# Performance work log

Measured on AMD Instinct MI355X. Metric: run time of the kernel, lower is better.

The kernel has to match this reference:

```python
import jax, jax.numpy as jnp
import numpy as np

B, R, M, L, H = 256, 2048, 65536, 64, 4  # batch, reservoir, memory_size, key_len, read_heads


def setup_inputs() -> dict:
    key = jax.random.key(0)
    ks = jax.random.split(key, 4)
    s = 1.0 / np.sqrt(R).astype(np.float32)  # ~xavier scale for Linear weights
    return {
        "reservoir_state": jax.random.normal(ks[0], (B, R), dtype=jnp.float32),
        "memory": jax.random.normal(ks[1], (1, M, L), dtype=jnp.float32),
        "Wk": jax.random.normal(ks[2], (H * L, R), dtype=jnp.float32) * s,
        "bk": jnp.zeros((H * L,), dtype=jnp.float32),
        "Wb": jax.random.normal(ks[3], (H, R), dtype=jnp.float32) * s,
        "bb": jnp.zeros((H,), dtype=jnp.float32),
    }


def reference(reservoir_state, memory, Wk, bk, Wb, bb):
    b = reservoir_state.shape[0]
    h = Wb.shape[0]
    # key projection -> [B, H, L]
    keys = (reservoir_state @ Wk.T + bk).reshape(b, h, -1)
    # per-head key strength, relu-gated -> [B, H]
    betas = jax.nn.relu(reservoir_state @ Wb.T + bb)
    # content addressing: dot(keys, memory rows) -> [B, H, M]
    dots = jnp.einsum('bhl,ml->bhm', keys, memory[0])
    # normalize by key norm (as in original: sqrt(sum(keys^2)))
    dots = dots / jnp.sqrt(jnp.sum(keys ** 2, axis=-1, keepdims=True))
    # beta-scaled softmax over memory slots
    return jax.nn.softmax(betas[:, :, None] * dots, axis=-1)
```

## Files before the change

### kernel.cpp

```cpp
#include <hip/hip_runtime.h>
#include <hip/hip_bf16.h>

#define BB   256
#define RR   2048
#define MM   65536
#define LL   64
#define HH   4
#define NROW 1024
#define KEYS 256

typedef float f32x4 __attribute__((ext_vector_type(4)));
typedef short short8 __attribute__((ext_vector_type(8)));

#define MFMA(A,B,C) __builtin_amdgcn_mfma_f32_16x16x32_bf16((A),(B),(C),0,0,0)

__device__ __forceinline__ unsigned short bf16_rn(float x) {
    union { float f; unsigned int u; } v; v.f = x;
    unsigned int r = v.u + 0x7FFFu + ((v.u >> 16) & 1u);
    return (unsigned short)(r >> 16);
}
__device__ __forceinline__ float bf16_to_f(unsigned short h) {
    union { float f; unsigned int u; } v; v.u = ((unsigned int)h) << 16; return v.f;
}
__device__ __forceinline__ void split8_store(const float* x, unsigned short* hi, unsigned short* lo) {
    unsigned int ph[4], pl[4];
#pragma unroll
    for (int j = 0; j < 4; ++j) {
        unsigned short h0 = bf16_rn(x[2*j]),   l0 = bf16_rn(x[2*j]   - bf16_to_f(h0));
        unsigned short h1 = bf16_rn(x[2*j+1]), l1 = bf16_rn(x[2*j+1] - bf16_to_f(h1));
        ph[j] = (unsigned int)h0 | ((unsigned int)h1 << 16);
        pl[j] = (unsigned int)l0 | ((unsigned int)l1 << 16);
    }
    ((uint4*)hi)[0] = make_uint4(ph[0], ph[1], ph[2], ph[3]);
    ((uint4*)lo)[0] = make_uint4(pl[0], pl[1], pl[2], pl[3]);
}

__global__ __launch_bounds__(256) void transpose_k(const float* __restrict__ in,
                                                   float* __restrict__ out,
                                                   int NR, int NC) {
    __shared__ float t[64 * 65];
    int r0 = blockIdx.x * 64, c0 = blockIdx.y * 64;
    int lane = threadIdx.x & 63, w = threadIdx.x >> 6;
#pragma unroll
    for (int i = 0; i < 16; ++i) {
        int rr = i * 4 + w;
        t[lane * 65 + rr] = in[(size_t)(r0 + rr) * NC + c0 + lane];
    }
    __syncthreads();
#pragma unroll
    for (int i = 0; i < 16; ++i) {
        int cc = i * 4 + w;
        out[(size_t)(c0 + cc) * NR + r0 + lane] = t[cc * 65 + lane];
    }
}

__global__ __launch_bounds__(256) void normmax_k(const float* __restrict__ mem,
                                                 float* __restrict__ normpart) {
    int row = blockIdx.x * 256 + threadIdx.x;
    const float4* p = (const float4*)(mem + (size_t)row * LL);
    float s = 0.f;
#pragma unroll
    for (int i = 0; i < 16; ++i) { float4 v = p[i]; s += v.x*v.x + v.y*v.y + v.z*v.z + v.w*v.w; }
    int lane = threadIdx.x & 63, w = threadIdx.x >> 6;
#pragma unroll
    for (int off = 1; off < 64; off <<= 1) s = fmaxf(s, __shfl_xor(s, off, 64));
    __shared__ float sm[4];
    if (lane == 0) sm[w] = s;
    __syncthreads();
    if (threadIdx.x == 0)
        normpart[blockIdx.x] = fmaxf(fmaxf(sm[0], sm[1]), fmaxf(sm[2], sm[3]));
}

__global__ __launch_bounds__(256) void prep_mem(const float* __restrict__ mem,
                                                unsigned short* __restrict__ bhi,
                                                unsigned short* __restrict__ blo) {
    int gid = blockIdx.x * 256 + threadIdx.x;
    int lane = gid & 63, frag = gid >> 6;
    int t = frag >> 1, c = frag & 1;
    int mrow = t * 16 + (lane & 15);
    int k0 = c * 32 + (lane >> 4) * 8;
    const float4* src = (const float4*)(mem + (size_t)mrow * LL + k0);
    float4 x0 = src[0], x1 = src[1];
    float x[8] = {x0.x, x0.y, x0.z, x0.w, x1.x, x1.y, x1.z, x1.w};
    split8_store(x, bhi + (size_t)gid * 8, blo + (size_t)gid * 8);
}

__global__ __launch_bounds__(256) void k0_keys(const float* __restrict__ S,
                                               const float* __restrict__ WkT,
                                               float* __restrict__ kpart) {
    __shared__ float sl[8 * 256];
    int bg = blockIdx.x, kc = blockIdx.y, tid = threadIdx.x;
    int b0 = bg * 8;
#pragma unroll
    for (int bi = 0; bi < 8; ++bi)
        sl[bi * 256 + tid] = S[(size_t)(b0 + bi) * RR + kc * 256 + tid];
    __syncthreads();
    float acc[8] = {0,0,0,0,0,0,0,0};
    const float* wp = WkT + (size_t)kc * 256 * KEYS + tid;
#pragma unroll 4
    for (int kk = 0; kk < 256; ++kk) {
        float wv = wp[kk * KEYS];
#pragma unroll
        for (int bi = 0; bi < 8; ++bi)
            acc[bi] = fmaf(sl[bi * 256 + kk], wv, acc[bi]);
    }
    float* op = kpart + (size_t)kc * BB * KEYS + (size_t)b0 * KEYS + tid;
#pragma unroll
    for (int bi = 0; bi < 8; ++bi)
        op[bi * KEYS] = acc[bi];
}

__global__ __launch_bounds__(256) void k1_finalize(const float* __restrict__ S,
                                                   const float* __restrict__ kpart,
                                                   const float* __restrict__ bk,
                                                   const float* __restrict__ Wb,
                                                   const float* __restrict__ bb,
                                                   const float* __restrict__ normpart,
                                                   float* __restrict__ q_rm,
                                                   float* __restrict__ brow) {
    int bh = blockIdx.x, b = bh >> 2, h = bh & 3;
    int tid = threadIdx.x, lane = tid & 63, w = tid >> 6;
    float p = 0.f;
#pragma unroll
    for (int i = 0; i < 8; ++i) {
        int k = i * 256 + tid;
        p += S[(size_t)b * RR + k] * Wb[(size_t)h * RR + k];
    }
    float nm = normpart[tid];
#pragma unroll
    for (int off = 1; off < 64; off <<= 1) {
        p  += __shfl_xor(p, off, 64);
        nm  = fmaxf(nm, __shfl_xor(nm, off, 64));
    }
    __shared__ float red[4], redm[4];
    if (lane == 0) { red[w] = p; redm[w] = nm; }
    __syncthreads();
    if (tid < 64) {
        float beta = red[0] + red[1] + red[2] + red[3] + bb[h];
        beta = fmaxf(beta, 0.f);
        float maxn = sqrtf(fmaxf(fmaxf(redm[0], redm[1]), fmaxf(redm[2], redm[3])));
        float kv = bk[h * LL + lane];
#pragma unroll
        for (int c = 0; c < 8; ++c)
            kv += kpart[(size_t)c * BB * KEYS + (size_t)b * KEYS + h * LL + lane];
        float sq = kv * kv;
#pragma unroll
        for (int off = 1; off < 64; off <<= 1) sq += __shfl_xor(sq, off, 64);
        float scale = beta / sqrtf(sq);
        q_rm[(size_t)bh * LL + lane] = kv * scale;
        if (lane == 0) brow[bh] = beta * maxn;
    }
}

__global__ __launch_bounds__(256) void prep_a(const float* __restrict__ q_rm,
                                              unsigned short* __restrict__ ahi,
                                              unsigned short* __restrict__ alo) {
    int gid = blockIdx.x * 256 + threadIdx.x;
    int lane = gid & 63, frag = gid >> 6;
    int rtg = frag >> 1, c = frag & 1;
    int row = rtg * 16 + (lane & 15);
    int k0 = c * 32 + (lane >> 4) * 8;
    const float4* src = (const float4*)(q_rm + (size_t)row * LL + k0);
    float4 x0 = src[0], x1 = src[1];
    float x[8] = {x0.x, x0.y, x0.z, x0.w, x1.x, x1.y, x1.z, x1.w};
    split8_store(x, ahi + (size_t)gid * 8, alo + (size_t)gid * 8);
}

__global__ __launch_bounds__(256) void k2_mfma(const unsigned short* __restrict__ bhi,
                                               const unsigned short* __restrict__ blo,
                                               const unsigned short* __restrict__ ahi,
                                               const unsigned short* __restrict__ alo,
                                               const float* __restrict__ brow,
                                               float* __restrict__ psum) {
    int bx = blockIdx.x;
    int mblk = bx >> 4, rg = bx & 15;
    int tid = threadIdx.x, w = tid >> 6, lane = tid & 63;
    int g = lane >> 4;
    short8 Ah[4][2], Al[4][2];
#pragma unroll
    for (int rt = 0; rt < 4; ++rt)
#pragma unroll
        for (int c = 0; c < 2; ++c) {
            size_t off = ((size_t)((rg * 4 + rt) * 2 + c) * 64 + lane) * 8;
            Ah[rt][c] = *(const short8*)(ahi + off);
            Al[rt][c] = *(const short8*)(alo + off);
        }
    float br[4][4];
#pragma unroll
    for (int rt = 0; rt < 4; ++rt)
#pragma unroll
        for (int r = 0; r < 4; ++r)
            br[rt][r] = brow[rg * 64 + rt * 16 + g * 4 + r];
    float s[4][4] = {{0.f}};
    int t0 = mblk * 64 + w * 16;
    for (int ti = 0; ti < 16; ++ti) {
        int t = t0 + ti;
        size_t o0 = ((size_t)(t * 2 + 0) * 64 + lane) * 8;
        size_t o1 = ((size_t)(t * 2 + 1) * 64 + lane) * 8;
        short8 Bh0 = *(const short8*)(bhi + o0);
        short8 Bh1 = *(const short8*)(bhi + o1);
        short8 Bl0 = *(const short8*)(blo + o0);
        short8 Bl1 = *(const short8*)(blo + o1);
#pragma unroll
        for (int rt = 0; rt < 4; ++rt) {
            f32x4 C = {0.f, 0.f, 0.f, 0.f};
            C = MFMA(Ah[rt][0], Bh0, C);
            C = MFMA(Ah[rt][1], Bh1, C);
            C = MFMA(Al[rt][0], Bh0, C);
            C = MFMA(Al[rt][1], Bh1, C);
            C = MFMA(Ah[rt][0], Bl0, C);
            C = MFMA(Ah[rt][1], Bl1, C);
#pragma unroll
            for (int r = 0; r < 4; ++r)
                s[rt][r] += __expf(C[r] - br[rt][r]);
        }
    }
#pragma unroll
    for (int rt = 0; rt < 4; ++rt)
#pragma unroll
        for (int r = 0; r < 4; ++r) {
            float v = s[rt][r];
            v += __shfl_xor(v, 1, 64);
            v += __shfl_xor(v, 2, 64);
            v += __shfl_xor(v, 4, 64);
            v += __shfl_xor(v, 8, 64);
            s[rt][r] = v;
        }
    if ((lane & 15) == 0) {
        int col = mblk * 4 + w;
#pragma unroll
        for (int rt = 0; rt < 4; ++rt)
#pragma unroll
            for (int r = 0; r < 4; ++r) {
                int row = rg * 64 + rt * 16 + g * 4 + r;
                psum[(size_t)row * 256 + col] = s[rt][r];
            }
    }
}

__global__ __launch_bounds__(256) void k3_combine(const float* __restrict__ psum,
                                                  float* __restrict__ ginv) {
    int row = blockIdx.x, tid = threadIdx.x, lane = tid & 63, w = tid >> 6;
    float v = psum[(size_t)row * 256 + tid];
#pragma unroll
    for (int off = 1; off < 64; off <<= 1) v += __shfl_xor(v, off, 64);
    __shared__ float sm[4];
    if (lane == 0) sm[w] = v;
    __syncthreads();
    if (tid == 0) ginv[row] = 1.0f / (sm[0] + sm[1] + sm[2] + sm[3]);
}

__global__ __launch_bounds__(256) void k4_mfma(const unsigned short* __restrict__ bhi,
                                               const unsigned short* __restrict__ blo,
                                               const unsigned short* __restrict__ ahi,
                                               const unsigned short* __restrict__ alo,
                                               const float* __restrict__ brow,
                                               const float* __restrict__ ginv,
                                               float* __restrict__ out) {
    int bx = blockIdx.x;
    int mblk = bx >> 4, rg = bx & 15;
    int tid = threadIdx.x, w = tid >> 6, lane = tid & 63;
    int g = lane >> 4;
    short8 Ah[4][2], Al[4][2];
#pragma unroll
    for (int rt = 0; rt < 4; ++rt)
#pragma unroll
        for (int c = 0; c < 2; ++c) {
            size_t off = ((size_t)((rg * 4 + rt) * 2 + c) * 64 + lane) * 8;
            Ah[rt][c] = *(const short8*)(ahi + off);
            Al[rt][c] = *(const short8*)(alo + off);
        }
    float br[4][4], gv[4][4];
    size_t rbase[4][4];
#pragma unroll
    for (int rt = 0; rt < 4; ++rt)
#pragma unroll
        for (int r = 0; r < 4; ++r) {
            int row = rg * 64 + rt * 16 + g * 4 + r;
            br[rt][r] = brow[row];
            gv[rt][r] = ginv[row];
            rbase[rt][r] = (size_t)row * MM + (lane & 15);
        }
    int t0 = mblk * 64 + w * 16;
    for (int ti = 0; ti < 16; ++ti) {
        int t = t0 + ti;
        size_t o0 = ((size_t)(t * 2 + 0) * 64 + lane) * 8;
        size_t o1 = ((size_t)(t * 2 + 1) * 64 + lane) * 8;
        short8 Bh0 = *(const short8*)(bhi + o0);
        short8 Bh1 = *(const short8*)(bhi + o1);
        short8 Bl0 = *(const short8*)(blo + o0);
        short8 Bl1 = *(const short8*)(blo + o1);
#pragma unroll
        for (int rt = 0; rt < 4; ++rt) {
            f32x4 C = {0.f, 0.f, 0.f, 0.f};
            C = MFMA(Ah[rt][0], Bh0, C);
            C = MFMA(Ah[rt][1], Bh1, C);
            C = MFMA(Al[rt][0], Bh0, C);
            C = MFMA(Al[rt][1], Bh1, C);
            C = MFMA(Ah[rt][0], Bl0, C);
            C = MFMA(Ah[rt][1], Bl1, C);
#pragma unroll
            for (int r = 0; r < 4; ++r) {
                float o = __expf(C[r] - br[rt][r]) * gv[rt][r];
                __builtin_nontemporal_store(o, out + rbase[rt][r] + (size_t)t * 16);
            }
        }
    }
}

extern "C" void kernel_launch(void* const* d_in, const int* in_sizes, int n_in,
                              void* d_out, int out_size, void* d_ws, size_t ws_size,
                              hipStream_t stream) {
    const float* S   = (const float*)d_in[0];
    const float* mem = (const float*)d_in[1];
    const float* Wk  = (const float*)d_in[2];
    const float* bk  = (const float*)d_in[3];
    const float* Wb  = (const float*)d_in[4];
    const float* bb  = (const float*)d_in[5];
    float* out = (float*)d_out;

    float* WkT      = (float*)d_ws;
    float* kpart    = WkT   + (size_t)RR * KEYS;
    float* q_rm     = kpart + (size_t)8 * BB * KEYS;
    float* psum     = q_rm  + (size_t)NROW * LL;
    float* brow     = psum  + (size_t)NROW * 256;
    float* ginv     = brow  + NROW;
    float* normpart = ginv  + NROW;
    unsigned short* bhi = (unsigned short*)(normpart + 256);
    unsigned short* blo = bhi + (size_t)8192 * 512;
    unsigned short* ahi = blo + (size_t)8192 * 512;
    unsigned short* alo = ahi + (size_t)128 * 512;

    transpose_k<<<dim3(BB / 64, RR / 64), 256, 0, stream>>>(Wk, WkT, KEYS, RR);
    normmax_k  <<<256,         256, 0, stream>>>(mem, normpart);
    prep_mem   <<<2048,        256, 0, stream>>>(mem, bhi, blo);
    k0_keys    <<<dim3(32, 8), 256, 0, stream>>>(S, WkT, kpart);
    k1_finalize<<<NROW,        256, 0, stream>>>(S, kpart, bk, Wb, bb, normpart, q_rm, brow);
    prep_a     <<<32,          256, 0, stream>>>(q_rm, ahi, alo);
    k2_mfma    <<<1024,        256, 0, stream>>>(bhi, blo, ahi, alo, brow, psum);
    k3_combine <<<NROW,        256, 0, stream>>>(psum, ginv);
    k4_mfma    <<<1024,        256, 0, stream>>>(bhi, blo, ahi, alo, brow, ginv, out);
}
```

Baseline: 397.3 us.

## Fuse norm-max into prep_mem, stage output via LDS, prefetch B, use exp2

```diff
diff --git a/kernel.cpp b/kernel.cpp
--- a/kernel.cpp
+++ b/kernel.cpp
@@ -13,6 +13,8 @@
 typedef short short8 __attribute__((ext_vector_type(8)));
 
 #define MFMA(A,B,C) __builtin_amdgcn_mfma_f32_16x16x32_bf16((A),(B),(C),0,0,0)
+#define LOG2E 1.4426950408889634f
+#define EXP2F(x) __builtin_amdgcn_exp2f(x)
 
 __device__ __forceinline__ unsigned short bf16_rn(float x) {
     union { float f; unsigned int u; } v; v.f = x;
@@ -54,35 +56,49 @@
     }
 }
 
-__global__ __launch_bounds__(256) void normmax_k(const float* __restrict__ mem,
-                                                 float* __restrict__ normpart) {
-    int row = blockIdx.x * 256 + threadIdx.x;
-    const float4* p = (const float4*)(mem + (size_t)row * LL);
-    float s = 0.f;
-#pragma unroll
-    for (int i = 0; i < 16; ++i) { float4 v = p[i]; s += v.x*v.x + v.y*v.y + v.z*v.z + v.w*v.w; }
-    int lane = threadIdx.x & 63, w = threadIdx.x >> 6;
-#pragma unroll
-    for (int off = 1; off < 64; off <<= 1) s = fmaxf(s, __shfl_xor(s, off, 64));
-    __shared__ float sm[4];
-    if (lane == 0) sm[w] = s;
-    __syncthreads();
-    if (threadIdx.x == 0)
-        normpart[blockIdx.x] = fmaxf(fmaxf(sm[0], sm[1]), fmaxf(sm[2], sm[3]));
-}
-
 __global__ __launch_bounds__(256) void prep_mem(const float* __restrict__ mem,
                                                 unsigned short* __restrict__ bhi,
-                                                unsigned short* __restrict__ blo) {
-    int gid = blockIdx.x * 256 + threadIdx.x;
-    int lane = gid & 63, frag = gid >> 6;
-    int t = frag >> 1, c = frag & 1;
-    int mrow = t * 16 + (lane & 15);
-    int k0 = c * 32 + (lane >> 4) * 8;
-    const float4* src = (const float4*)(mem + (size_t)mrow * LL + k0);
-    float4 x0 = src[0], x1 = src[1];
-    float x[8] = {x0.x, x0.y, x0.z, x0.w, x1.x, x1.y, x1.z, x1.w};
-    split8_store(x, bhi + (size_t)gid * 8, blo + (size_t)gid * 8);
+                                                unsigned short* __restrict__ blo,
+                                                float* __restrict__ normpart) {
+    __shared__ float t[128 * 68];
+    __shared__ float rowsq[128];
+    int blk = blockIdx.x, tid = threadIdx.x;
+    const f32x4* src = (const f32x4*)(mem + (size_t)blk * 128 * LL);
+#pragma unroll
+    for (int i = 0; i < 8; ++i) {
+        int idx = i * 256 + tid;
+        int row = idx >> 4, c4 = idx & 15;
+        *(f32x4*)&t[row * 68 + c4 * 4] = src[idx];
+    }
+    __syncthreads();
+    if (tid < 128) {
+        const float* rp = t + tid * 68;
+        float s = 0.f;
+#pragma unroll
+        for (int k = 0; k < 64; ++k) s = fmaf(rp[k], rp[k], s);
+        rowsq[tid] = s;
+    }
+    __syncthreads();
+    if (tid < 64) {
+        float m = fmaxf(rowsq[tid], rowsq[tid + 64]);
+#pragma unroll
+        for (int off = 1; off < 64; off <<= 1) m = fmaxf(m, __shfl_xor(m, off, 64));
+        if (tid == 0) normpart[blk] = m;
+    }
+#pragma unroll
+    for (int i = 0; i < 4; ++i) {
+        int slot = i * 256 + tid;
+        int lane = slot & 63, frag_l = slot >> 6;
+        int t_l = frag_l >> 1, c = frag_l & 1;
+        int row = t_l * 16 + (lane & 15);
+        int k0 = c * 32 + (lane >> 4) * 8;
+        const float* p = t + row * 68 + k0;
+        float x[8];
+#pragma unroll
+        for (int j = 0; j < 8; ++j) x[j] = p[j];
+        size_t gslot = ((size_t)blk * 16 + frag_l) * 64 + lane;
+        split8_store(x, bhi + gslot * 8, blo + gslot * 8);
+    }
 }
 
 __global__ __launch_bounds__(256) void k0_keys(const float* __restrict__ S,
@@ -126,7 +142,7 @@
         int k = i * 256 + tid;
         p += S[(size_t)b * RR + k] * Wb[(size_t)h * RR + k];
     }
-    float nm = normpart[tid];
+    float nm = fmaxf(normpart[tid], normpart[256 + tid]);
 #pragma unroll
     for (int off = 1; off < 64; off <<= 1) {
         p  += __shfl_xor(p, off, 64);
@@ -146,9 +162,9 @@
         float sq = kv * kv;
 #pragma unroll
         for (int off = 1; off < 64; off <<= 1) sq += __shfl_xor(sq, off, 64);
-        float scale = beta / sqrtf(sq);
+        float scale = beta * LOG2E / sqrtf(sq);
         q_rm[(size_t)bh * LL + lane] = kv * scale;
-        if (lane == 0) brow[bh] = beta * maxn;
+        if (lane == 0) brow[bh] = beta * maxn * LOG2E;
     }
 }
 
@@ -166,14 +182,18 @@
     split8_store(x, ahi + (size_t)gid * 8, alo + (size_t)gid * 8);
 }
 
+__device__ __forceinline__ void decode_wg(int bx, int& mblk, int& rg) {
+    int wg = ((bx & 7) << 7) | (bx >> 3);
+    mblk = wg >> 4; rg = wg & 15;
+}
+
 __global__ __launch_bounds__(256) void k2_mfma(const unsigned short* __restrict__ bhi,
                                                const unsigned short* __restrict__ blo,
                                                const unsigned short* __restrict__ ahi,
                                                const unsigned short* __restrict__ alo,
                                                const float* __restrict__ brow,
                                                float* __restrict__ psum) {
-    int bx = blockIdx.x;
-    int mblk = bx >> 4, rg = bx & 15;
+    int mblk, rg; decode_wg(blockIdx.x, mblk, rg);
     int tid = threadIdx.x, w = tid >> 6, lane = tid & 63;
     int g = lane >> 4;
     short8 Ah[4][2], Al[4][2];
@@ -193,14 +213,20 @@
             br[rt][r] = brow[rg * 64 + rt * 16 + g * 4 + r];
     float s[4][4] = {{0.f}};
     int t0 = mblk * 64 + w * 16;
+    short8 Bh0, Bh1, Bl0, Bl1;
+    {
+        size_t o = (size_t)t0 * 1024 + (size_t)lane * 8;
+        Bh0 = *(const short8*)(bhi + o); Bh1 = *(const short8*)(bhi + o + 512);
+        Bl0 = *(const short8*)(blo + o); Bl1 = *(const short8*)(blo + o + 512);
+    }
+#pragma unroll 4
     for (int ti = 0; ti < 16; ++ti) {
-        int t = t0 + ti;
-        size_t o0 = ((size_t)(t * 2 + 0) * 64 + lane) * 8;
-        size_t o1 = ((size_t)(t * 2 + 1) * 64 + lane) * 8;
-        short8 Bh0 = *(const short8*)(bhi + o0);
-        short8 Bh1 = *(const short8*)(bhi + o1);
-        short8 Bl0 = *(const short8*)(blo + o0);
-        short8 Bl1 = *(const short8*)(blo + o1);
+        int tn = t0 + ((ti < 15) ? ti + 1 : 15);
+        size_t on = (size_t)tn * 1024 + (size_t)lane * 8;
+        short8 nh0 = *(const short8*)(bhi + on);
+        short8 nh1 = *(const short8*)(bhi + on + 512);
+        short8 nl0 = *(const short8*)(blo + on);
+        short8 nl1 = *(const short8*)(blo + on + 512);
 #pragma unroll
         for (int rt = 0; rt < 4; ++rt) {
             f32x4 C = {0.f, 0.f, 0.f, 0.f};
@@ -212,8 +238,9 @@
             C = MFMA(Ah[rt][1], Bl1, C);
 #pragma unroll
             for (int r = 0; r < 4; ++r)
-                s[rt][r] += __expf(C[r] - br[rt][r]);
-        }
+                s[rt][r] += EXP2F(C[r] - br[rt][r]);
+        }
+        Bh0 = nh0; Bh1 = nh1; Bl0 = nl0; Bl1 = nl1;
     }
 #pragma unroll
     for (int rt = 0; rt < 4; ++rt)
@@ -257,10 +284,11 @@
                                                const float* __restrict__ brow,
                                                const float* __restrict__ ginv,
                                                float* __restrict__ out) {
-    int bx = blockIdx.x;
-    int mblk = bx >> 4, rg = bx & 15;
+    __shared__ float ot[4][64 * 20];
+    int mblk, rg; decode_wg(blockIdx.x, mblk, rg);
     int tid = threadIdx.x, w = tid >> 6, lane = tid & 63;
     int g = lane >> 4;
+    float* wt = &ot[w][0];
     short8 Ah[4][2], Al[4][2];
 #pragma unroll
     for (int rt = 0; rt < 4; ++rt)
@@ -271,7 +299,6 @@
             Al[rt][c] = *(const short8*)(alo + off);
         }
     float br[4][4], gv[4][4];
-    size_t rbase[4][4];
 #pragma unroll
     for (int rt = 0; rt < 4; ++rt)
 #pragma unroll
@@ -279,17 +306,23 @@
             int row = rg * 64 + rt * 16 + g * 4 + r;
             br[rt][r] = brow[row];
             gv[rt][r] = ginv[row];
-            rbase[rt][r] = (size_t)row * MM + (lane & 15);
         }
     int t0 = mblk * 64 + w * 16;
+    short8 Bh0, Bh1, Bl0, Bl1;
+    {
+        size_t o = (size_t)t0 * 1024 + (size_t)lane * 8;
+        Bh0 = *(const short8*)(bhi + o); Bh1 = *(const short8*)(bhi + o + 512);
+        Bl0 = *(const short8*)(blo + o); Bl1 = *(const short8*)(blo + o + 512);
+    }
+#pragma unroll 2
     for (int ti = 0; ti < 16; ++ti) {
         int t = t0 + ti;
-        size_t o0 = ((size_t)(t * 2 + 0) * 64 + lane) * 8;
-        size_t o1 = ((size_t)(t * 2 + 1) * 64 + lane) * 8;
-        short8 Bh0 = *(const short8*)(bhi + o0);
-        short8 Bh1 = *(const short8*)(bhi + o1);
-        short8 Bl0 = *(const short8*)(blo + o0);
-        short8 Bl1 = *(const short8*)(blo + o1);
+        int tn = t0 + ((ti < 15) ? ti + 1 : 15);
+        size_t on = (size_t)tn * 1024 + (size_t)lane * 8;
+        short8 nh0 = *(const short8*)(bhi + on);
+        short8 nh1 = *(const short8*)(bhi + on + 512);
+        short8 nl0 = *(const short8*)(blo + on);
+        short8 nl1 = *(const short8*)(blo + on + 512);
 #pragma unroll
         for (int rt = 0; rt < 4; ++rt) {
             f32x4 C = {0.f, 0.f, 0.f, 0.f};
@@ -300,11 +333,18 @@
             C = MFMA(Ah[rt][0], Bl0, C);
             C = MFMA(Ah[rt][1], Bl1, C);
 #pragma unroll
-            for (int r = 0; r < 4; ++r) {
-                float o = __expf(C[r] - br[rt][r]) * gv[rt][r];
-                __builtin_nontemporal_store(o, out + rbase[rt][r] + (size_t)t * 16);
-            }
-        }
+            for (int r = 0; r < 4; ++r)
+                wt[(rt * 16 + g * 4 + r) * 20 + (lane & 15)] =
+                    EXP2F(C[r] - br[rt][r]) * gv[rt][r];
+        }
+#pragma unroll
+        for (int j = 0; j < 4; ++j) {
+            int rl = j * 16 + (lane >> 2);
+            f32x4 v = *(const f32x4*)&wt[rl * 20 + (lane & 3) * 4];
+            float* dst = out + (size_t)(rg * 64 + rl) * MM + (size_t)t * 16 + (lane & 3) * 4;
+            __builtin_nontemporal_store(v, (f32x4*)dst);
+        }
+        Bh0 = nh0; Bh1 = nh1; Bl0 = nl0; Bl1 = nl1;
     }
 }
 
@@ -326,14 +366,13 @@
     float* brow     = psum  + (size_t)NROW * 256;
     float* ginv     = brow  + NROW;
     float* normpart = ginv  + NROW;
-    unsigned short* bhi = (unsigned short*)(normpart + 256);
+    unsigned short* bhi = (unsigned short*)(normpart + 512);
     unsigned short* blo = bhi + (size_t)8192 * 512;
     unsigned short* ahi = blo + (size_t)8192 * 512;
     unsigned short* alo = ahi + (size_t)128 * 512;
 
     transpose_k<<<dim3(BB / 64, RR / 64), 256, 0, stream>>>(Wk, WkT, KEYS, RR);
-    normmax_k  <<<256,         256, 0, stream>>>(mem, normpart);
-    prep_mem   <<<2048,        256, 0, stream>>>(mem, bhi, blo);
+    prep_mem   <<<512,         256, 0, stream>>>(mem, bhi, blo, normpart);
     k0_keys    <<<dim3(32, 8), 256, 0, stream>>>(S, WkT, kpart);
     k1_finalize<<<NROW,        256, 0, stream>>>(S, kpart, bk, Wb, bb, normpart, q_rm, brow);
     prep_a     <<<32,          256, 0, stream>>>(q_rm, ahi, alo);
```

Result: no change. 395.6 us (-0.4%).
